# Kernel optimization log

Measured on AMD Instinct MI355X. Metric: run time of the kernel, lower is better.

The kernel has to match this reference:

```python
import jax, jax.numpy as jnp
import numpy as np

N_NODES = 100000
N_EDGES = 1600000
IN_F = 128
HID_F = 128
OUT_F = 16
N_GRAPHS = 256


def setup_inputs() -> dict:
    key = jax.random.key(0)
    ks = jax.random.split(key, 6)
    x = jax.random.normal(ks[0], (N_NODES, IN_F), dtype=jnp.float32)
    W1 = jax.random.normal(ks[1], (IN_F, HID_F), dtype=jnp.float32) * (1.0 / np.sqrt(IN_F))
    b1 = jax.random.normal(ks[2], (HID_F,), dtype=jnp.float32) * 0.01
    W2 = jax.random.normal(ks[3], (HID_F, OUT_F), dtype=jnp.float32) * (1.0 / np.sqrt(HID_F))
    b2 = jax.random.normal(ks[4], (OUT_F,), dtype=jnp.float32) * 0.01
    edge_index = jax.random.randint(ks[5], (2, N_EDGES), 0, N_NODES, dtype=jnp.int32)
    # sorted segment ids covering all graphs (~N/G nodes per graph, none empty)
    batch = ((jnp.arange(N_NODES, dtype=jnp.int64) * N_GRAPHS) // N_NODES).astype(jnp.int32)
    return {"x": x, "W1": W1, "b1": b1, "W2": W2, "b2": b2,
            "edge_index": edge_index, "batch": batch, "num_graphs": N_GRAPHS}


def gcn_conv(x, W, b, edge_index):
    # PyG GCNConv: h = x @ W; add self-loops; norm = deg^-1/2[src] * deg^-1/2[dst];
    # out[dst] += norm * h[src]; out += bias
    n = x.shape[0]
    h = x @ W  # [N, H]
    loop = jnp.arange(n, dtype=edge_index.dtype)
    src = jnp.concatenate([edge_index[0], loop])
    dst = jnp.concatenate([edge_index[1], loop])
    deg = jax.ops.segment_sum(jnp.ones_like(dst, dtype=h.dtype), dst, num_segments=n)
    dinv = jnp.where(deg > 0, jax.lax.rsqrt(jnp.maximum(deg, 1.0)), 0.0)
    norm = dinv[src] * dinv[dst]  # [E+N]
    msg = h[src] * norm[:, None]  # gather + scale
    out = jax.ops.segment_sum(msg, dst, num_segments=n)  # scatter-add
    return out + b


def reference(x, W1, b1, W2, b2, edge_index, batch, num_graphs):
    h = gcn_conv(x, W1, b1, edge_index)
    h = jax.nn.relu(h)
    pooled = jax.ops.segment_max(h, batch, num_segments=num_graphs)  # global max pool
    logits = pooled @ W2 + b2
    return jax.nn.log_softmax(logits, axis=-1)
```

## Files before the change

kernel.cpp:

```cpp
#include <hip/hip_runtime.h>

#define N_NODES 100000
#define N_EDGES 1600000
#define FDIM 128
#define OUTF 16
#define NGRAPH 256

#define NBLK 512
#define CHUNK 3125
#define NB_BUCKET 391
#define BC_N (NB_BUCKET * NBLK)
#define BC_SCAN_NB 196

typedef unsigned int uint;
typedef unsigned short ushort;
typedef short bf16x8 __attribute__((ext_vector_type(8)));
typedef float f32x4 __attribute__((ext_vector_type(4)));

__device__ inline uint pack_bf16(float a, float b) {
    uint ua = __float_as_uint(a); ua = (ua + 0x7fffu + ((ua >> 16) & 1u)) >> 16;
    uint ub = __float_as_uint(b); ub = (ub + 0x7fffu + ((ub >> 16) & 1u)) >> 16;
    return ua | (ub << 16);
}
__device__ inline ushort bf16_1(float a) {
    uint u = __float_as_uint(a);
    return (ushort)((u + 0x7fffu + ((u >> 16) & 1u)) >> 16);
}
__device__ inline void unpack_bf16(uint v, float& a, float& b) {
    a = __uint_as_float(v << 16);
    b = __uint_as_float(v & 0xffff0000u);
}

__global__ void k_zero(float* __restrict__ pooled, int* __restrict__ row_start) {
    int i = blockIdx.x * 256 + threadIdx.x;
    if (i < NGRAPH * FDIM) pooled[i] = 0.0f;
    if (i == 0) row_start[N_NODES] = N_EDGES;
}

__launch_bounds__(256)
__global__ void k_bhist(const int* __restrict__ dst, int* __restrict__ bcount) {
    __shared__ int hist[NB_BUCKET];
    int t = threadIdx.x, blk = blockIdx.x;
    for (int i = t; i < NB_BUCKET; i += 256) hist[i] = 0;
    __syncthreads();
    int base = blk * CHUNK;
    for (int j = t; j < CHUNK; j += 256) atomicAdd(&hist[dst[base + j] >> 8], 1);
    __syncthreads();
    for (int i = t; i < NB_BUCKET; i += 256) bcount[i * NBLK + blk] = hist[i];
}

__global__ void k_scan1g(const int* __restrict__ in, int* __restrict__ offs,
                         int* __restrict__ bsums, int n) {
    __shared__ int tmp[256];
    int t = threadIdx.x;
    int base = blockIdx.x * 1024 + t * 4;
    int c[4]; int s = 0;
#pragma unroll
    for (int j = 0; j < 4; ++j) { c[j] = (base + j < n) ? in[base + j] : 0; s += c[j]; }
    tmp[t] = s; __syncthreads();
    for (int off = 1; off < 256; off <<= 1) {
        int v = (t >= off) ? tmp[t - off] : 0;
        __syncthreads();
        tmp[t] += v;
        __syncthreads();
    }
    int run = tmp[t] - s;
#pragma unroll
    for (int j = 0; j < 4; ++j) { if (base + j < n) offs[base + j] = run; run += c[j]; }
    if (t == 255) bsums[blockIdx.x] = tmp[255];
}

__global__ void k_scan2g(int* __restrict__ bsums, int* __restrict__ offs,
                         int nb, int n, int total) {
    if (threadIdx.x == 0) {
        int acc = 0;
        for (int i = 0; i < nb; ++i) { int v = bsums[i]; bsums[i] = acc; acc += v; }
        offs[n] = total;
    }
}

__global__ void k_scan3g(int* __restrict__ offs, const int* __restrict__ bsums, int n) {
    int t = threadIdx.x;
    int base = blockIdx.x * 1024 + t * 4;
    int add = bsums[blockIdx.x];
#pragma unroll
    for (int j = 0; j < 4; ++j) if (base + j < n) offs[base + j] += add;
}

__launch_bounds__(256)
__global__ void k_bucket(const int* __restrict__ src, const int* __restrict__ dst,
                         const int* __restrict__ boff, int2* __restrict__ ebuf) {
    __shared__ int cur[NB_BUCKET];
    int t = threadIdx.x, blk = blockIdx.x;
    for (int i = t; i < NB_BUCKET; i += 256) cur[i] = boff[i * NBLK + blk];
    __syncthreads();
    int base = blk * CHUNK;
    for (int j = t; j < CHUNK; j += 256) {
        int d = dst[base + j], s = src[base + j];
        int pos = atomicAdd(&cur[d >> 8], 1);
        ebuf[pos] = make_int2(d, s);
    }
}

__launch_bounds__(256)
__global__ void k_build(const int2* __restrict__ ebuf, const int* __restrict__ boff,
                        int* __restrict__ row_start, float* __restrict__ dinv,
                        int* __restrict__ csr_src) {
    __shared__ int cnt[256], sh[256], cur[256];
    int t = threadIdx.x, b = blockIdx.x;
    int bstart = boff[b * NBLK];
    int bend   = boff[(b + 1) * NBLK];
    cnt[t] = 0;
    __syncthreads();
    for (int j = bstart + t; j < bend; j += 256)
        atomicAdd(&cnt[ebuf[j].x & 255], 1);
    __syncthreads();
    int c = cnt[t];
    sh[t] = c;
    __syncthreads();
    for (int o = 1; o < 256; o <<= 1) {
        int v = (t >= o) ? sh[t - o] : 0;
        __syncthreads();
        sh[t] += v;
        __syncthreads();
    }
    int rs = bstart + sh[t] - c;
    cur[t] = rs;
    int node = b * 256 + t;
    if (node < N_NODES) {
        row_start[node] = rs;
        dinv[node] = rsqrtf((float)c + 1.0f);
    }
    __syncthreads();
    for (int j = bstart + t; j < bend; j += 256) {
        int2 e = ebuf[j];
        int pos = atomicAdd(&cur[e.x & 255], 1);
        csr_src[pos] = e.y;
    }
}

__global__ void k_wcast(const float* __restrict__ W, ushort* __restrict__ wt) {
    int i = blockIdx.x * 256 + threadIdx.x;
    int col = i >> 7, k = i & 127;
    wt[col * 128 + k] = bf16_1(W[k * 128 + col]);
}

#define BM 128
#define LDP 136
__launch_bounds__(256)
__global__ void k_gemm(const float* __restrict__ x, const ushort* __restrict__ wt,
                       ushort* __restrict__ hbf) {
    __shared__ ushort AL[BM][LDP];
    __shared__ ushort WL[128][LDP];
    int t = threadIdx.x;
    int r0 = blockIdx.x * BM;

    for (int i = t; i < 128 * 16; i += 256) {
        int r = i >> 4, s = i & 15;
        *(uint4*)&WL[r][s * 8] = *(const uint4*)&wt[r * 128 + s * 8];
    }
    {
        int r = t >> 1, half = t & 1;
        int grow = r0 + r; if (grow >= N_NODES) grow = N_NODES - 1;
        const float4* xp = (const float4*)(x + (long)grow * FDIM + half * 64);
        ushort* ap = &AL[r][half * 64];
#pragma unroll
        for (int i = 0; i < 16; ++i) {
            float4 v = xp[i];
            uint2 p;
            p.x = pack_bf16(v.x, v.y);
            p.y = pack_bf16(v.z, v.w);
            *(uint2*)&ap[i * 4] = p;
        }
    }
    __syncthreads();

    int w = t >> 6, l = t & 63;
    int lr = l & 15;
    int lk = (l >> 4) * 8;
    f32x4 acc[2][8] = {};
#pragma unroll
    for (int kc = 0; kc < 4; ++kc) {
        int ko = kc * 32 + lk;
        bf16x8 a0 = *(const bf16x8*)&AL[w * 32 + lr][ko];
        bf16x8 a1 = *(const bf16x8*)&AL[w * 32 + 16 + lr][ko];
        bf16x8 b[8];
#pragma unroll
        for (int ct = 0; ct < 8; ++ct) b[ct] = *(const bf16x8*)&WL[ct * 16 + lr][ko];
#pragma unroll
        for (int ct = 0; ct < 8; ++ct) {
            acc[0][ct] = __builtin_amdgcn_mfma_f32_16x16x32_bf16(a0, b[ct], acc[0][ct], 0, 0, 0);
            acc[1][ct] = __builtin_amdgcn_mfma_f32_16x16x32_bf16(a1, b[ct], acc[1][ct], 0, 0, 0);
        }
    }
    int rbase = r0 + w * 32 + (l >> 4) * 4;
#pragma unroll
    for (int rt = 0; rt < 2; ++rt) {
#pragma unroll
        for (int ct = 0; ct < 8; ++ct) {
#pragma unroll
            for (int reg = 0; reg < 4; ++reg) {
                int row = rbase + rt * 16 + reg;
                if (row < N_NODES)
                    hbf[(long)row * FDIM + ct * 16 + lr] = bf16_1(acc[rt][ct][reg]);
            }
        }
    }
}

__launch_bounds__(256)
__global__ void k_agg(const ushort* __restrict__ hbf, const float* __restrict__ dinv,
                      const int* __restrict__ row_start, const int* __restrict__ csr_src,
                      const float* __restrict__ b1, ushort* __restrict__ outbf) {
    int t = threadIdx.x;
    int lane = t & 31;
    int node = blockIdx.x * 8 + (t >> 5);
    const uint2* hb = (const uint2*)hbf;
    float dd = dinv[node];
    uint2 v = hb[node * 32 + lane];
    float f0, f1, f2, f3;
    unpack_bf16(v.x, f0, f1); unpack_bf16(v.y, f2, f3);
    float s0 = dd * f0, s1 = dd * f1, s2 = dd * f2, s3 = dd * f3;
    int beg = row_start[node], end = row_start[node + 1];
    int j = beg;
    for (; j + 1 < end; j += 2) {
        int sa = csr_src[j], sb = csr_src[j + 1];
        float da = dinv[sa], db = dinv[sb];
        uint2 va = hb[sa * 32 + lane];
        uint2 vb = hb[sb * 32 + lane];
        float a0, a1, a2, a3, c0, c1, c2, c3;
        unpack_bf16(va.x, a0, a1); unpack_bf16(va.y, a2, a3);
        unpack_bf16(vb.x, c0, c1); unpack_bf16(vb.y, c2, c3);
        s0 += da * a0 + db * c0;
        s1 += da * a1 + db * c1;
        s2 += da * a2 + db * c2;
        s3 += da * a3 + db * c3;
    }
    if (j < end) {
        int sa = csr_src[j];
        float da = dinv[sa];
        uint2 va = hb[sa * 32 + lane];
        float a0, a1, a2, a3;
        unpack_bf16(va.x, a0, a1); unpack_bf16(va.y, a2, a3);
        s0 += da * a0; s1 += da * a1; s2 += da * a2; s3 += da * a3;
    }
    float4 bv = ((const float4*)b1)[lane];
    uint2 o;
    o.x = pack_bf16(dd * s0 + bv.x, dd * s1 + bv.y);
    o.y = pack_bf16(dd * s2 + bv.z, dd * s3 + bv.w);
    ((uint2*)outbf)[node * 32 + lane] = o;
}

#define PNODES 64
__global__ void k_pool2(const ushort* __restrict__ outbf, const int* __restrict__ batch,
                        float* __restrict__ pooled) {
    int f = threadIdx.x;
    int r0 = blockIdx.x * PNODES;
    if (r0 >= N_NODES) return;
    int end = r0 + PNODES; if (end > N_NODES) end = N_NODES;
    float m = 0.0f;
    int gcur = batch[r0];
    for (int i = r0; i < end; ++i) {
        int g = batch[i];
        if (g != gcur) {
            atomicMax((int*)&pooled[gcur * FDIM + f], __float_as_int(m));
            m = 0.0f; gcur = g;
        }
        uint u = outbf[(long)i * FDIM + f];
        m = fmaxf(m, __uint_as_float(u << 16));
    }
    atomicMax((int*)&pooled[gcur * FDIM + f], __float_as_int(m));
}

__global__ void k_head(const float* __restrict__ pooled, const float* __restrict__ W2,
                       const float* __restrict__ b2, float* __restrict__ out) {
    int g = blockIdx.x;
    int lane = threadIdx.x;
    int c = lane & 15;
    float acc = b2[c];
    for (int k = 0; k < FDIM; ++k) acc += pooled[g * FDIM + k] * W2[k * OUTF + c];
    float m = acc;
    for (int off = 1; off < 16; off <<= 1) m = fmaxf(m, __shfl_xor(m, off, 16));
    float s = expf(acc - m);
    for (int off = 1; off < 16; off <<= 1) s += __shfl_xor(s, off, 16);
    if (lane < 16) out[g * OUTF + c] = acc - m - logf(s);
}

extern "C" void kernel_launch(void* const* d_in, const int* in_sizes, int n_in,
                              void* d_out, int out_size, void* d_ws, size_t ws_size,
                              hipStream_t stream) {
    const float* x  = (const float*)d_in[0];
    const float* W1 = (const float*)d_in[1];
    const float* b1 = (const float*)d_in[2];
    const float* W2 = (const float*)d_in[3];
    const float* b2 = (const float*)d_in[4];
    const int* ei   = (const int*)d_in[5];
    const int* batch = (const int*)d_in[6];
    const int* src = ei;
    const int* dst = ei + N_EDGES;
    float* out = (float*)d_out;

    char* ws = (char*)d_ws;
    float*  dinv      = (float*) (ws + 0);
    int*    row_start = (int*)   (ws + 400000);
    float*  pooled    = (float*) (ws + 800064);
    int*    bcount    = (int*)   (ws + 931200);
    int*    boff      = (int*)   (ws + 1732032);
    int*    bsums     = (int*)   (ws + 2532864);
    int*    csr_src   = (int*)   (ws + 2533696);
    int2*   ebuf      = (int2*)  (ws + 8933696);
    ushort* hbf       = (ushort*)(ws + 21733696);
    ushort* outbf     = (ushort*)(ws + 47333696);
    ushort* wtbf      = (ushort*)(ws + 72933696);

    k_zero   <<<128, 256, 0, stream>>>(pooled, row_start);
    k_bhist  <<<NBLK, 256, 0, stream>>>(dst, bcount);
    k_scan1g <<<BC_SCAN_NB, 256, 0, stream>>>(bcount, boff, bsums, BC_N);
    k_scan2g <<<1, 64, 0, stream>>>(bsums, boff, BC_SCAN_NB, BC_N, N_EDGES);
    k_scan3g <<<BC_SCAN_NB, 256, 0, stream>>>(boff, bsums, BC_N);
    k_bucket <<<NBLK, 256, 0, stream>>>(src, dst, boff, ebuf);
    k_build  <<<NB_BUCKET, 256, 0, stream>>>(ebuf, boff, row_start, dinv, csr_src);
    k_wcast  <<<64, 256, 0, stream>>>(W1, wtbf);
    k_gemm   <<<(N_NODES + BM - 1) / BM, 256, 0, stream>>>(x, wtbf, hbf);
    k_agg    <<<N_NODES / 8, 256, 0, stream>>>(hbf, dinv, row_start, csr_src, b1, outbf);
    k_pool2  <<<(N_NODES + PNODES - 1) / PNODES, FDIM, 0, stream>>>(outbf, batch, pooled);
    k_head   <<<NGRAPH, 64, 0, stream>>>(pooled, W2, b2, out);
}
```

Measured before the change: 296.2 us.

## Prescale h by dinv in GEMM, pack edge buffer, fuse setup kernels

```diff
diff --git a/kernel.cpp b/kernel.cpp
--- a/kernel.cpp
+++ b/kernel.cpp
@@ -6,11 +6,11 @@
 #define OUTF 16
 #define NGRAPH 256
 
-#define NBLK 512
-#define CHUNK 3125
+#define NBLK 256
+#define CHUNK 6250
 #define NB_BUCKET 391
 #define BC_N (NB_BUCKET * NBLK)
-#define BC_SCAN_NB 196
+#define BC_SCAN_NB 98
 
 typedef unsigned int uint;
 typedef unsigned short ushort;
@@ -31,16 +31,19 @@
     b = __uint_as_float(v & 0xffff0000u);
 }
 
-__global__ void k_zero(float* __restrict__ pooled, int* __restrict__ row_start) {
-    int i = blockIdx.x * 256 + threadIdx.x;
-    if (i < NGRAPH * FDIM) pooled[i] = 0.0f;
-    if (i == 0) row_start[N_NODES] = N_EDGES;
-}
-
-__launch_bounds__(256)
-__global__ void k_bhist(const int* __restrict__ dst, int* __restrict__ bcount) {
+__launch_bounds__(256)
+__global__ void k_bhist(const int* __restrict__ dst, int* __restrict__ bcount,
+                        float* __restrict__ pooled, int* __restrict__ row_start,
+                        const float* __restrict__ W, ushort* __restrict__ wt) {
     __shared__ int hist[NB_BUCKET];
     int t = threadIdx.x, blk = blockIdx.x;
+    int gi = blk * 256 + t;
+    if (gi < NGRAPH * FDIM) pooled[gi] = 0.0f;
+    if (gi < FDIM * FDIM) {
+        int col = gi >> 7, k = gi & 127;
+        wt[col * 128 + k] = bf16_1(W[k * 128 + col]);
+    }
+    if (gi == 0) row_start[N_NODES] = N_EDGES;
     for (int i = t; i < NB_BUCKET; i += 256) hist[i] = 0;
     __syncthreads();
     int base = blk * CHUNK;
@@ -89,7 +92,7 @@
 
 __launch_bounds__(256)
 __global__ void k_bucket(const int* __restrict__ src, const int* __restrict__ dst,
-                         const int* __restrict__ boff, int2* __restrict__ ebuf) {
+                         const int* __restrict__ boff, uint* __restrict__ ebuf) {
     __shared__ int cur[NB_BUCKET];
     int t = threadIdx.x, blk = blockIdx.x;
     for (int i = t; i < NB_BUCKET; i += 256) cur[i] = boff[i * NBLK + blk];
@@ -98,12 +101,12 @@
     for (int j = t; j < CHUNK; j += 256) {
         int d = dst[base + j], s = src[base + j];
         int pos = atomicAdd(&cur[d >> 8], 1);
-        ebuf[pos] = make_int2(d, s);
-    }
-}
-
-__launch_bounds__(256)
-__global__ void k_build(const int2* __restrict__ ebuf, const int* __restrict__ boff,
+        ebuf[pos] = ((uint)(d & 255) << 17) | (uint)s;
+    }
+}
+
+__launch_bounds__(256)
+__global__ void k_build(const uint* __restrict__ ebuf, const int* __restrict__ boff,
                         int* __restrict__ row_start, float* __restrict__ dinv,
                         int* __restrict__ csr_src) {
     __shared__ int cnt[256], sh[256], cur[256];
@@ -113,7 +116,7 @@
     cnt[t] = 0;
     __syncthreads();
     for (int j = bstart + t; j < bend; j += 256)
-        atomicAdd(&cnt[ebuf[j].x & 255], 1);
+        atomicAdd(&cnt[ebuf[j] >> 17], 1);
     __syncthreads();
     int c = cnt[t];
     sh[t] = c;
@@ -133,23 +136,17 @@
     }
     __syncthreads();
     for (int j = bstart + t; j < bend; j += 256) {
-        int2 e = ebuf[j];
-        int pos = atomicAdd(&cur[e.x & 255], 1);
-        csr_src[pos] = e.y;
-    }
-}
-
-__global__ void k_wcast(const float* __restrict__ W, ushort* __restrict__ wt) {
-    int i = blockIdx.x * 256 + threadIdx.x;
-    int col = i >> 7, k = i & 127;
-    wt[col * 128 + k] = bf16_1(W[k * 128 + col]);
+        uint e = ebuf[j];
+        int pos = atomicAdd(&cur[e >> 17], 1);
+        csr_src[pos] = (int)(e & 0x1FFFFu);
+    }
 }
 
 #define BM 128
 #define LDP 136
 __launch_bounds__(256)
 __global__ void k_gemm(const float* __restrict__ x, const ushort* __restrict__ wt,
-                       ushort* __restrict__ hbf) {
+                       const float* __restrict__ dinv, ushort* __restrict__ hbf) {
     __shared__ ushort AL[BM][LDP];
     __shared__ ushort WL[128][LDP];
     int t = threadIdx.x;
@@ -197,12 +194,13 @@
 #pragma unroll
     for (int rt = 0; rt < 2; ++rt) {
 #pragma unroll
-        for (int ct = 0; ct < 8; ++ct) {
-#pragma unroll
-            for (int reg = 0; reg < 4; ++reg) {
-                int row = rbase + rt * 16 + reg;
-                if (row < N_NODES)
-                    hbf[(long)row * FDIM + ct * 16 + lr] = bf16_1(acc[rt][ct][reg]);
+        for (int reg = 0; reg < 4; ++reg) {
+            int row = rbase + rt * 16 + reg;
+            if (row < N_NODES) {
+                float dv = dinv[row];
+#pragma unroll
+                for (int ct = 0; ct < 8; ++ct)
+                    hbf[(long)row * FDIM + ct * 16 + lr] = bf16_1(dv * acc[rt][ct][reg]);
             }
         }
     }
@@ -216,34 +214,33 @@
     int lane = t & 31;
     int node = blockIdx.x * 8 + (t >> 5);
     const uint2* hb = (const uint2*)hbf;
-    float dd = dinv[node];
     uint2 v = hb[node * 32 + lane];
-    float f0, f1, f2, f3;
-    unpack_bf16(v.x, f0, f1); unpack_bf16(v.y, f2, f3);
-    float s0 = dd * f0, s1 = dd * f1, s2 = dd * f2, s3 = dd * f3;
+    float s0, s1, s2, s3;
+    unpack_bf16(v.x, s0, s1); unpack_bf16(v.y, s2, s3);
     int beg = row_start[node], end = row_start[node + 1];
     int j = beg;
-    for (; j + 1 < end; j += 2) {
-        int sa = csr_src[j], sb = csr_src[j + 1];
-        float da = dinv[sa], db = dinv[sb];
-        uint2 va = hb[sa * 32 + lane];
-        uint2 vb = hb[sb * 32 + lane];
-        float a0, a1, a2, a3, c0, c1, c2, c3;
-        unpack_bf16(va.x, a0, a1); unpack_bf16(va.y, a2, a3);
-        unpack_bf16(vb.x, c0, c1); unpack_bf16(vb.y, c2, c3);
-        s0 += da * a0 + db * c0;
-        s1 += da * a1 + db * c1;
-        s2 += da * a2 + db * c2;
-        s3 += da * a3 + db * c3;
-    }
-    if (j < end) {
-        int sa = csr_src[j];
-        float da = dinv[sa];
-        uint2 va = hb[sa * 32 + lane];
+    for (; j + 3 < end; j += 4) {
+        uint2 va = hb[csr_src[j] * 32 + lane];
+        uint2 vb = hb[csr_src[j + 1] * 32 + lane];
+        uint2 vc = hb[csr_src[j + 2] * 32 + lane];
+        uint2 vd = hb[csr_src[j + 3] * 32 + lane];
         float a0, a1, a2, a3;
         unpack_bf16(va.x, a0, a1); unpack_bf16(va.y, a2, a3);
-        s0 += da * a0; s1 += da * a1; s2 += da * a2; s3 += da * a3;
-    }
+        s0 += a0; s1 += a1; s2 += a2; s3 += a3;
+        unpack_bf16(vb.x, a0, a1); unpack_bf16(vb.y, a2, a3);
+        s0 += a0; s1 += a1; s2 += a2; s3 += a3;
+        unpack_bf16(vc.x, a0, a1); unpack_bf16(vc.y, a2, a3);
+        s0 += a0; s1 += a1; s2 += a2; s3 += a3;
+        unpack_bf16(vd.x, a0, a1); unpack_bf16(vd.y, a2, a3);
+        s0 += a0; s1 += a1; s2 += a2; s3 += a3;
+    }
+    for (; j < end; ++j) {
+        uint2 va = hb[csr_src[j] * 32 + lane];
+        float a0, a1, a2, a3;
+        unpack_bf16(va.x, a0, a1); unpack_bf16(va.y, a2, a3);
+        s0 += a0; s1 += a1; s2 += a2; s3 += a3;
+    }
+    float dd = dinv[node];
     float4 bv = ((const float4*)b1)[lane];
     uint2 o;
     o.x = pack_bf16(dd * s0 + bv.x, dd * s1 + bv.y);
@@ -305,23 +302,21 @@
     int*    row_start = (int*)   (ws + 400000);
     float*  pooled    = (float*) (ws + 800064);
     int*    bcount    = (int*)   (ws + 931200);
-    int*    boff      = (int*)   (ws + 1732032);
-    int*    bsums     = (int*)   (ws + 2532864);
-    int*    csr_src   = (int*)   (ws + 2533696);
-    int2*   ebuf      = (int2*)  (ws + 8933696);
-    ushort* hbf       = (ushort*)(ws + 21733696);
-    ushort* outbf     = (ushort*)(ws + 47333696);
-    ushort* wtbf      = (ushort*)(ws + 72933696);
-
-    k_zero   <<<128, 256, 0, stream>>>(pooled, row_start);
-    k_bhist  <<<NBLK, 256, 0, stream>>>(dst, bcount);
+    int*    boff      = (int*)   (ws + 1331648);
+    int*    bsums     = (int*)   (ws + 1732096);
+    int*    csr_src   = (int*)   (ws + 1732544);
+    uint*   ebuf      = (uint*)  (ws + 8132544);
+    ushort* hbf       = (ushort*)(ws + 14532544);
+    ushort* outbf     = (ushort*)(ws + 40132544);
+    ushort* wtbf      = (ushort*)(ws + 65732544);
+
+    k_bhist  <<<NBLK, 256, 0, stream>>>(dst, bcount, pooled, row_start, W1, wtbf);
     k_scan1g <<<BC_SCAN_NB, 256, 0, stream>>>(bcount, boff, bsums, BC_N);
     k_scan2g <<<1, 64, 0, stream>>>(bsums, boff, BC_SCAN_NB, BC_N, N_EDGES);
     k_scan3g <<<BC_SCAN_NB, 256, 0, stream>>>(boff, bsums, BC_N);
     k_bucket <<<NBLK, 256, 0, stream>>>(src, dst, boff, ebuf);
     k_build  <<<NB_BUCKET, 256, 0, stream>>>(ebuf, boff, row_start, dinv, csr_src);
-    k_wcast  <<<64, 256, 0, stream>>>(W1, wtbf);
-    k_gemm   <<<(N_NODES + BM - 1) / BM, 256, 0, stream>>>(x, wtbf, hbf);
+    k_gemm   <<<(N_NODES + BM - 1) / BM, 256, 0, stream>>>(x, wtbf, dinv, hbf);
     k_agg    <<<N_NODES / 8, 256, 0, stream>>>(hbf, dinv, row_start, csr_src, b1, outbf);
     k_pool2  <<<(N_NODES + PNODES - 1) / PNODES, FDIM, 0, stream>>>(outbf, batch, pooled);
     k_head   <<<NGRAPH, 64, 0, stream>>>(pooled, W2, b2, out);
```

Result: faster. 276.1 us (-6.8%).
